# Optimization experiments

Hardware: AMD Instinct MI355X
Metric: run time of the kernel (lower is better)

Reference implementation:

```python
import jax, jax.numpy as jnp
import numpy as np

EPS = 1e-7  # K.epsilon()
ATTN_WIDTH = 12
B, L, D = 8, 4096, 768


def setup_inputs() -> dict:
    key = jax.random.key(0)
    k1, k2 = jax.random.split(key)
    x = jax.random.normal(k1, (B, L, D), dtype=jnp.float32)
    Wa = jax.random.normal(k2, (D, 1), dtype=jnp.float32) * 0.05  # RandomNormal(stddev=0.05)
    return {"x": x, "Wa": Wa}


def reference(x, Wa):
    """Banded rank-1 self-attention.

    e[b,i,j] = u[b,i]*u[b,j] with u = x @ Wa, masked to the trailing band
    i-w+1 <= j <= i, normalized by the row sum (+eps), then v = a @ x.
    Because e is rank-1 inside the band, we never materialize the LxL matrix:
      wsum_i  = sum_{j=i-w+1}^{i} u_j          (windowed cumsum)
      wvec_i  = sum_{j=i-w+1}^{i} u_j * x_j    (windowed cumsum of u*x)
      v_i     = u_i * wvec_i / (u_i * wsum_i + eps)
    which is exactly e/(sum(e)+eps) @ x.
    """
    w = ATTN_WIDTH
    u = jnp.einsum('bld,do->bl', x, Wa)            # [B, L]
    cu = jnp.cumsum(u, axis=1)                      # [B, L]
    cux = jnp.cumsum(u[..., None] * x, axis=1)      # [B, L, D]
    # shifted[i] = cu[i-w] (0 for i < w)
    cu_shift = jnp.pad(cu, ((0, 0), (w, 0)))[:, :L]
    cux_shift = jnp.pad(cux, ((0, 0), (w, 0), (0, 0)))[:, :L, :]
    wsum = cu - cu_shift                            # [B, L]
    wvec = cux - cux_shift                          # [B, L, D]
    denom = u * wsum + EPS                          # [B, L]
    v = (u[..., None] * wvec) / denom[..., None]    # [B, L, D]
    return v
```

## Files before the change

### kernel.cpp

```cpp
#include <hip/hip_runtime.h>

typedef float vfloat4 __attribute__((ext_vector_type(4)));

namespace {
constexpr int kB = 8;
constexpr int kL = 4096;
constexpr int kD = 768;
constexpr int kW = 12;
constexpr int kHalo = kW - 1;
constexpr float kEps = 1e-7f;

constexpr int kT = 16;
constexpr int kRows = kT + kHalo;
constexpr int kThreads = 192;
constexpr int kChunks = kL / kT;
constexpr int kGrid = kB * kChunks;
}

__global__ __launch_bounds__(kThreads, 3) void fused_banded_kernel(
    const float* __restrict__ x, const float* __restrict__ Wa,
    float* __restrict__ out) {
  __shared__ double s_ud[kRows];
  __shared__ float s_uf[kRows];
  __shared__ float s_scale[kT];

  const int blk = blockIdx.x;
  const int b = blk / kChunks;
  const int i0 = (blk % kChunks) * kT;
  const float* xb = x + (size_t)b * kL * kD;
  float* ob = out + (size_t)b * kL * kD;
  const int tid = threadIdx.x;
  const int lane = tid & 63;
  const int wv = tid >> 6;

  vfloat4 w[3];
#pragma unroll
  for (int k = 0; k < 3; ++k)
    w[k] = *(const vfloat4*)(Wa + 4 * lane + 256 * k);

  if (i0 >= kHalo) {
    vfloat4 xv[9][3];
#pragma unroll
    for (int it = 0; it < 9; ++it) {
      const int row = i0 - kHalo + wv + 3 * it;
#pragma unroll
      for (int k = 0; k < 3; ++k)
        xv[it][k] = *(const vfloat4*)(xb + (size_t)row * kD + 4 * lane + 256 * k);
    }
    double p[9];
#pragma unroll
    for (int it = 0; it < 9; ++it) {
      double q = 0.0;
#pragma unroll
      for (int k = 0; k < 3; ++k) {
        q += (double)xv[it][k].x * (double)w[k].x + (double)xv[it][k].y * (double)w[k].y +
             (double)xv[it][k].z * (double)w[k].z + (double)xv[it][k].w * (double)w[k].w;
      }
      p[it] = q;
    }
#pragma unroll
    for (int s = 32; s >= 1; s >>= 1) {
#pragma unroll
      for (int it = 0; it < 9; ++it) p[it] += __shfl_xor(p[it], s, 64);
    }
    if (lane == 0) {
#pragma unroll
      for (int it = 0; it < 9; ++it) {
        const int lr = wv + 3 * it;
        s_ud[lr] = p[it];
        s_uf[lr] = (float)p[it];
      }
    }
  } else {
#pragma unroll
    for (int it = 0; it < 9; ++it) {
      const int lr = wv + 3 * it;
      const int row = i0 - kHalo + lr;
      double p = 0.0;
      if (row >= 0) {
        vfloat4 xv[3];
#pragma unroll
        for (int k = 0; k < 3; ++k)
          xv[k] = *(const vfloat4*)(xb + (size_t)row * kD + 4 * lane + 256 * k);
#pragma unroll
        for (int k = 0; k < 3; ++k) {
          p += (double)xv[k].x * (double)w[k].x + (double)xv[k].y * (double)w[k].y +
               (double)xv[k].z * (double)w[k].z + (double)xv[k].w * (double)w[k].w;
        }
#pragma unroll
        for (int s = 32; s >= 1; s >>= 1) p += __shfl_xor(p, s, 64);
      }
      if (lane == 0) {
        s_ud[lr] = p;
        s_uf[lr] = (float)p;
      }
    }
  }
  __syncthreads();

  float uf[kRows];
#pragma unroll
  for (int r = 0; r < kRows; ++r) uf[r] = s_uf[r];

  if (tid < kT) {
    double wsum = 0.0;
#pragma unroll
    for (int k = 0; k < kW; ++k) wsum += s_ud[tid + k];
    const double uu = s_ud[tid + kHalo];
    s_scale[tid] = (float)(uu / (uu * wsum + (double)kEps));
  }

  const int c0 = 4 * tid;
  vfloat4 ring[kW];
#pragma unroll
  for (int r = 0; r < kHalo; ++r) {
    const int row = i0 - kHalo + r;
    vfloat4 v = {0.f, 0.f, 0.f, 0.f};
    if (row >= 0) v = *(const vfloat4*)(xb + (size_t)row * kD + c0);
    ring[r] = v;
  }
  __syncthreads();

  float sc[kT];
#pragma unroll
  for (int t = 0; t < kT; ++t) sc[t] = s_scale[t];

#pragma unroll
  for (int t = 0; t < kT; ++t) {
    const int i = i0 + t;
    const int r = kHalo + t;
    ring[r % kW] = *(const vfloat4*)(xb + (size_t)i * kD + c0);
    vfloat4 acc = {0.f, 0.f, 0.f, 0.f};
#pragma unroll
    for (int j = 0; j < kW; ++j) {
      const float uu = uf[r - j];
      const vfloat4 xv = ring[(r - j) % kW];
      acc.x += uu * xv.x; acc.y += uu * xv.y;
      acc.z += uu * xv.z; acc.w += uu * xv.w;
    }
    const float s = sc[t];
    vfloat4 o = {s * acc.x, s * acc.y, s * acc.z, s * acc.w};
    __builtin_nontemporal_store(o, (vfloat4*)(ob + (size_t)i * kD + c0));
  }
}

extern "C" void kernel_launch(void* const* d_in, const int* in_sizes, int n_in,
                              void* d_out, int out_size, void* d_ws, size_t ws_size,
                              hipStream_t stream) {
  const float* x = (const float*)d_in[0];
  const float* Wa = (const float*)d_in[1];
  float* out = (float*)d_out;
  (void)d_ws; (void)ws_size;

  fused_banded_kernel<<<kGrid, kThreads, 0, stream>>>(x, Wa, out);
}
```

Baseline: 198.7 us.

## Load x tile once into registers and compute dot products from it

Each thread now loads its 4-column slice of all 27 rows (tile plus halo) into registers once. It computes partial u dot products from those registers, reduces them through a two-step shuffle plus a shared-memory partial table, and reuses the same registers for the banded accumulation. This removes the second global read of x, which the old kernel needed because u was computed with a different thread-to-column mapping. In exchange the block holds 27 vec4 values per thread, adds an extra barrier and a shared-memory reduction, and may put pressure on registers and occupancy.

```diff
diff --git a/kernel.cpp b/kernel.cpp
--- a/kernel.cpp
+++ b/kernel.cpp
@@ -15,13 +15,14 @@
 constexpr int kThreads = 192;
 constexpr int kChunks = kL / kT;
 constexpr int kGrid = kB * kChunks;
+constexpr int kGroups = kThreads / 4;
 }
 
-__global__ __launch_bounds__(kThreads, 3) void fused_banded_kernel(
+__global__ __launch_bounds__(kThreads, 3) void fused_onepass_kernel(
     const float* __restrict__ x, const float* __restrict__ Wa,
     float* __restrict__ out) {
+  __shared__ double s_part[kRows][kGroups + 1];
   __shared__ double s_ud[kRows];
-  __shared__ float s_uf[kRows];
   __shared__ float s_scale[kT];
 
   const int blk = blockIdx.x;
@@ -30,77 +31,47 @@
   const float* xb = x + (size_t)b * kL * kD;
   float* ob = out + (size_t)b * kL * kD;
   const int tid = threadIdx.x;
-  const int lane = tid & 63;
-  const int wv = tid >> 6;
+  const int c0 = 4 * tid;
 
-  vfloat4 w[3];
+  const vfloat4 w4 = *(const vfloat4*)(Wa + c0);
+
+  vfloat4 xr[kRows];
+  if (i0 >= kHalo) {
 #pragma unroll
-  for (int k = 0; k < 3; ++k)
-    w[k] = *(const vfloat4*)(Wa + 4 * lane + 256 * k);
-
-  if (i0 >= kHalo) {
-    vfloat4 xv[9][3];
-#pragma unroll
-    for (int it = 0; it < 9; ++it) {
-      const int row = i0 - kHalo + wv + 3 * it;
-#pragma unroll
-      for (int k = 0; k < 3; ++k)
-        xv[it][k] = *(const vfloat4*)(xb + (size_t)row * kD + 4 * lane + 256 * k);
-    }
-    double p[9];
-#pragma unroll
-    for (int it = 0; it < 9; ++it) {
-      double q = 0.0;
-#pragma unroll
-      for (int k = 0; k < 3; ++k) {
-        q += (double)xv[it][k].x * (double)w[k].x + (double)xv[it][k].y * (double)w[k].y +
-             (double)xv[it][k].z * (double)w[k].z + (double)xv[it][k].w * (double)w[k].w;
-      }
-      p[it] = q;
-    }
-#pragma unroll
-    for (int s = 32; s >= 1; s >>= 1) {
-#pragma unroll
-      for (int it = 0; it < 9; ++it) p[it] += __shfl_xor(p[it], s, 64);
-    }
-    if (lane == 0) {
-#pragma unroll
-      for (int it = 0; it < 9; ++it) {
-        const int lr = wv + 3 * it;
-        s_ud[lr] = p[it];
-        s_uf[lr] = (float)p[it];
-      }
-    }
+    for (int r = 0; r < kRows; ++r)
+      xr[r] = *(const vfloat4*)(xb + (size_t)(i0 - kHalo + r) * kD + c0);
   } else {
 #pragma unroll
-    for (int it = 0; it < 9; ++it) {
-      const int lr = wv + 3 * it;
-      const int row = i0 - kHalo + lr;
-      double p = 0.0;
-      if (row >= 0) {
-        vfloat4 xv[3];
+    for (int r = 0; r < kRows; ++r) {
+      const int row = i0 - kHalo + r;
+      vfloat4 v = {0.f, 0.f, 0.f, 0.f};
+      if (row >= 0) v = *(const vfloat4*)(xb + (size_t)row * kD + c0);
+      xr[r] = v;
+    }
+  }
+
 #pragma unroll
-        for (int k = 0; k < 3; ++k)
-          xv[k] = *(const vfloat4*)(xb + (size_t)row * kD + 4 * lane + 256 * k);
-#pragma unroll
-        for (int k = 0; k < 3; ++k) {
-          p += (double)xv[k].x * (double)w[k].x + (double)xv[k].y * (double)w[k].y +
-               (double)xv[k].z * (double)w[k].z + (double)xv[k].w * (double)w[k].w;
-        }
-#pragma unroll
-        for (int s = 32; s >= 1; s >>= 1) p += __shfl_xor(p, s, 64);
-      }
-      if (lane == 0) {
-        s_ud[lr] = p;
-        s_uf[lr] = (float)p;
-      }
-    }
+  for (int r = 0; r < kRows; ++r) {
+    double p = (double)xr[r].x * (double)w4.x + (double)xr[r].y * (double)w4.y +
+               (double)xr[r].z * (double)w4.z + (double)xr[r].w * (double)w4.w;
+    p += __shfl_xor(p, 1, 64);
+    p += __shfl_xor(p, 2, 64);
+    if ((tid & 3) == 0) s_part[r][tid >> 2] = p;
   }
   __syncthreads();
 
-  float uf[kRows];
+  if (tid < kRows) {
+    double a0 = 0.0, a1 = 0.0, a2 = 0.0, a3 = 0.0;
 #pragma unroll
-  for (int r = 0; r < kRows; ++r) uf[r] = s_uf[r];
+    for (int g = 0; g < kGroups; g += 4) {
+      a0 += s_part[tid][g + 0];
+      a1 += s_part[tid][g + 1];
+      a2 += s_part[tid][g + 2];
+      a3 += s_part[tid][g + 3];
+    }
+    s_ud[tid] = (a0 + a1) + (a2 + a3);
+  }
+  __syncthreads();
 
   if (tid < kT) {
     double wsum = 0.0;
@@ -110,37 +81,25 @@
     s_scale[tid] = (float)(uu / (uu * wsum + (double)kEps));
   }
 
-  const int c0 = 4 * tid;
-  vfloat4 ring[kW];
+  float uf[kRows];
 #pragma unroll
-  for (int r = 0; r < kHalo; ++r) {
-    const int row = i0 - kHalo + r;
-    vfloat4 v = {0.f, 0.f, 0.f, 0.f};
-    if (row >= 0) v = *(const vfloat4*)(xb + (size_t)row * kD + c0);
-    ring[r] = v;
-  }
+  for (int r = 0; r < kRows; ++r) uf[r] = (float)s_ud[r];
   __syncthreads();
-
-  float sc[kT];
-#pragma unroll
-  for (int t = 0; t < kT; ++t) sc[t] = s_scale[t];
 
 #pragma unroll
   for (int t = 0; t < kT; ++t) {
-    const int i = i0 + t;
-    const int r = kHalo + t;
-    ring[r % kW] = *(const vfloat4*)(xb + (size_t)i * kD + c0);
     vfloat4 acc = {0.f, 0.f, 0.f, 0.f};
 #pragma unroll
     for (int j = 0; j < kW; ++j) {
-      const float uu = uf[r - j];
-      const vfloat4 xv = ring[(r - j) % kW];
+      const int r = kHalo + t - j;
+      const float uu = uf[r];
+      const vfloat4 xv = xr[r];
       acc.x += uu * xv.x; acc.y += uu * xv.y;
       acc.z += uu * xv.z; acc.w += uu * xv.w;
     }
-    const float s = sc[t];
+    const float s = s_scale[t];
     vfloat4 o = {s * acc.x, s * acc.y, s * acc.z, s * acc.w};
-    __builtin_nontemporal_store(o, (vfloat4*)(ob + (size_t)i * kD + c0));
+    __builtin_nontemporal_store(o, (vfloat4*)(ob + (size_t)(i0 + t) * kD + c0));
   }
 }
 
@@ -152,5 +111,5 @@
   float* out = (float*)d_out;
   (void)d_ws; (void)ws_size;
 
-  fused_banded_kernel<<<kGrid, kThreads, 0, stream>>>(x, Wa, out);
+  fused_onepass_kernel<<<kGrid, kThreads, 0, stream>>>(x, Wa, out);
 }
```

New measurement: 184.4 us. 7.2% less time.
